# Kernel tuning notes

Hardware: AMD Instinct MI355X
Metric: run time of the kernel (lower is better)

Reference implementation:

```python
import jax, jax.numpy as jnp
import numpy as np

KSIZE = 8
STRIDE = 4
HEADS = 8
DIM_HEAD = 32
EPS = 1e-5


def _layernorm(x, g, b):
    m = jnp.mean(x, axis=-1, keepdims=True)
    v = jnp.mean(jnp.square(x - m), axis=-1, keepdims=True)
    return (x - m) / jnp.sqrt(v + EPS) * g + b


def setup_inputs() -> dict:
    key = jax.random.key(0)
    ks = jax.random.split(key, 4)
    B, H, W, C = 8, 64, 64, 256
    inner = HEADS * DIM_HEAD  # 256
    x = jax.random.normal(ks[0], (B, H, W, C), dtype=jnp.float32)
    return {
        "x": x,
        "ln1_g": jnp.ones((C,), jnp.float32),
        "ln1_b": jnp.zeros((C,), jnp.float32),
        "ln2_g": jnp.ones((C,), jnp.float32),
        "ln2_b": jnp.zeros((C,), jnp.float32),
        "w_qkv": jax.random.normal(ks[1], (C, inner * 3), jnp.float32) * 0.02,
        "w_out": jax.random.normal(ks[2], (inner, C), jnp.float32) * 0.02,
        "b_out": jnp.zeros((C,), jnp.float32),
    }


def reference(x, ln1_g, ln1_b, ln2_g, ln2_b, w_qkv, w_out, b_out):
    B, H, W, C = x.shape
    k, s = KSIZE, STRIDE
    nH = (H - k) // s + 1
    nW = (W - k) // s + 1
    L = nH * nW
    n = k * k  # tokens per window

    # window index grids (im2col / unfold)
    rows = jnp.arange(nH)[:, None] * s + jnp.arange(k)[None, :]  # [nH, k]
    cols = jnp.arange(nW)[:, None] * s + jnp.arange(k)[None, :]  # [nW, k]
    ridx = rows[:, None, :, None]  # [nH,1,k,1]
    cidx = cols[None, :, None, :]  # [1,nW,1,k]

    # unfold: [B, nH, nW, k, k, C] -> [(B L), (k k), C]
    patches = x[:, ridx, cidx, :].reshape(B * L, n, C)

    # LocalAttention2D.norm then AttentionBlock.norm
    p = _layernorm(patches, ln1_g, ln1_b)
    h = _layernorm(p, ln2_g, ln2_b)

    qkv = h @ w_qkv  # [(B L), n, 3*inner]
    q, kk, v = jnp.split(qkv, 3, axis=-1)
    q = q.reshape(B * L, n, HEADS, DIM_HEAD)
    kk = kk.reshape(B * L, n, HEADS, DIM_HEAD)
    v = v.reshape(B * L, n, HEADS, DIM_HEAD)

    scale = DIM_HEAD ** -0.5
    dots = jnp.einsum('bnhd,bmhd->bhnm', q, kk) * scale
    attn = jax.nn.softmax(dots, axis=-1)
    o = jnp.einsum('bhnm,bmhd->bnhd', attn, v).reshape(B * L, n, HEADS * DIM_HEAD)
    o = o @ w_out + b_out  # [(B L), n, C]

    # fold (col2im overlap-add)
    o = o.reshape(B, nH, nW, k, k, C)
    out = jnp.zeros((B, H, W, C), x.dtype).at[:, ridx, cidx, :].add(o)

    # normalization: fold(unfold(ones)) == overlap counts
    counts = jnp.zeros((H, W), x.dtype).at[ridx, cidx].add(1.0)
    return out / counts[None, :, :, None]
```

## Files before the change

### kernel.cpp

```cpp
#include <hip/hip_runtime.h>
#include <hip/hip_bf16.h>
#include <cstdint>
#include <cstddef>

#define LN_EPS 1e-5f
#define B_    8
#define HW_   64
#define C_    256
#define NTOK  (B_ * HW_ * HW_)
#define HEADS_ 8
#define DH_    32
#define NPATCH 15

__global__ __launch_bounds__(256) void ln_stats_kernel(
    const float* __restrict__ x, const float* __restrict__ g1,
    const float* __restrict__ b1, float4* __restrict__ stats)
{
    const int gid  = blockIdx.x * 256 + threadIdx.x;
    const int tok  = gid >> 6;
    const int lane = gid & 63;
    if (tok >= NTOK) return;
    const float4 xv = reinterpret_cast<const float4*>(x + (size_t)tok * C_)[lane];
    float s  = xv.x + xv.y + xv.z + xv.w;
    float sq = xv.x*xv.x + xv.y*xv.y + xv.z*xv.z + xv.w*xv.w;
    for (int off = 32; off; off >>= 1) {
        s  += __shfl_xor(s, off);
        sq += __shfl_xor(sq, off);
    }
    const float m1 = s * (1.0f / 256.0f);
    const float r1 = rsqrtf(fmaxf(sq * (1.0f / 256.0f) - m1 * m1, 0.0f) + LN_EPS);
    const float4 g = reinterpret_cast<const float4*>(g1)[lane];
    const float4 b = reinterpret_cast<const float4*>(b1)[lane];
    const float y0 = (xv.x - m1) * r1 * g.x + b.x;
    const float y1 = (xv.y - m1) * r1 * g.y + b.y;
    const float y2 = (xv.z - m1) * r1 * g.z + b.z;
    const float y3 = (xv.w - m1) * r1 * g.w + b.w;
    float s2  = y0 + y1 + y2 + y3;
    float sq2 = y0*y0 + y1*y1 + y2*y2 + y3*y3;
    for (int off = 32; off; off >>= 1) {
        s2  += __shfl_xor(s2, off);
        sq2 += __shfl_xor(sq2, off);
    }
    const float m2 = s2 * (1.0f / 256.0f);
    const float r2 = rsqrtf(fmaxf(sq2 * (1.0f / 256.0f) - m2 * m2, 0.0f) + LN_EPS);
    if (lane == 0) stats[tok] = make_float4(m1, r1, m2, r2);
}

__global__ __launch_bounds__(256) void qkv_kernel(
    const float* __restrict__ x, const float4* __restrict__ stats,
    const float* __restrict__ g1, const float* __restrict__ b1,
    const float* __restrict__ g2, const float* __restrict__ b2,
    const float* __restrict__ w, float* __restrict__ qkv)
{
    __shared__ float At[16][72];
    __shared__ float Bt[16][64];
    const int tid  = threadIdx.x;
    const int tok0 = blockIdx.y * 64;
    const int n0   = blockIdx.x * 64;
    const int ty = tid >> 4, tx = tid & 15;
    const int st = tid >> 2, sseg = tid & 3;
    const int bk = tid >> 4, bx = tid & 15;
    const float4 s4 = stats[tok0 + st];
    const float* xrow = x + (size_t)(tok0 + st) * C_;
    float acc[4][4] = {};
    for (int kk = 0; kk < 16; ++kk) {
        const int k0 = kk * 16;
        const int ka = k0 + sseg * 4;
        const float4 xv  = *reinterpret_cast<const float4*>(xrow + ka);
        const float4 g1v = *reinterpret_cast<const float4*>(g1 + ka);
        const float4 b1v = *reinterpret_cast<const float4*>(b1 + ka);
        const float4 g2v = *reinterpret_cast<const float4*>(g2 + ka);
        const float4 b2v = *reinterpret_cast<const float4*>(b2 + ka);
        const float h0 = ((xv.x - s4.x)*s4.y*g1v.x + b1v.x - s4.z)*s4.w*g2v.x + b2v.x;
        const float h1 = ((xv.y - s4.x)*s4.y*g1v.y + b1v.y - s4.z)*s4.w*g2v.y + b2v.y;
        const float h2 = ((xv.z - s4.x)*s4.y*g1v.z + b1v.z - s4.z)*s4.w*g2v.z + b2v.z;
        const float h3 = ((xv.w - s4.x)*s4.y*g1v.w + b1v.w - s4.z)*s4.w*g2v.w + b2v.w;
        const float4 wv = *reinterpret_cast<const float4*>(w + (size_t)(k0 + bk) * 768 + n0 + bx * 4);
        __syncthreads();
        At[sseg*4+0][st] = h0;
        At[sseg*4+1][st] = h1;
        At[sseg*4+2][st] = h2;
        At[sseg*4+3][st] = h3;
        *reinterpret_cast<float4*>(&Bt[bk][bx*4]) = wv;
        __syncthreads();
        #pragma unroll
        for (int k = 0; k < 16; ++k) {
            const float4 a = *reinterpret_cast<const float4*>(&At[k][ty*4]);
            const float4 b = *reinterpret_cast<const float4*>(&Bt[k][tx*4]);
            acc[0][0] += a.x*b.x; acc[0][1] += a.x*b.y; acc[0][2] += a.x*b.z; acc[0][3] += a.x*b.w;
            acc[1][0] += a.y*b.x; acc[1][1] += a.y*b.y; acc[1][2] += a.y*b.z; acc[1][3] += a.y*b.w;
            acc[2][0] += a.z*b.x; acc[2][1] += a.z*b.y; acc[2][2] += a.z*b.z; acc[2][3] += a.z*b.w;
            acc[3][0] += a.w*b.x; acc[3][1] += a.w*b.y; acc[3][2] += a.w*b.z; acc[3][3] += a.w*b.w;
        }
    }
    #pragma unroll
    for (int r = 0; r < 4; ++r) {
        const float4 o = make_float4(acc[r][0], acc[r][1], acc[r][2], acc[r][3]);
        *reinterpret_cast<float4*>(qkv + (size_t)(tok0 + ty*4 + r) * 768 + n0 + tx*4) = o;
    }
}

__global__ __launch_bounds__(256) void attn_o_kernel(
    const float* __restrict__ qkv, float* __restrict__ obuf)
{
    __shared__ float q_lds[64][36];
    __shared__ float kT[32][68];
    __shared__ float v_lds[64][36];
    __shared__ float p_lds[64][68];
    const int tid = threadIdx.x;
    const int b  = blockIdx.y;
    const int hd = blockIdx.z;
    const int pi = blockIdx.x / NPATCH;
    const int pj = blockIdx.x % NPATCH;
    const int t = tid >> 2, seg = tid & 3;
    const int pr = t >> 3, pc = t & 7;
    const size_t pixbase = ((size_t)((b * 64 + 4*pi + pr) * 64) + (4*pj + pc));
    {
        const size_t base = pixbase * 768 + hd * 32 + seg * 8;
        const float4 qa = *reinterpret_cast<const float4*>(qkv + base);
        const float4 qb = *reinterpret_cast<const float4*>(qkv + base + 4);
        const float4 ka = *reinterpret_cast<const float4*>(qkv + base + 256);
        const float4 kb = *reinterpret_cast<const float4*>(qkv + base + 260);
        const float4 va = *reinterpret_cast<const float4*>(qkv + base + 512);
        const float4 vb = *reinterpret_cast<const float4*>(qkv + base + 516);
        *reinterpret_cast<float4*>(&q_lds[t][seg*8    ]) = qa;
        *reinterpret_cast<float4*>(&q_lds[t][seg*8 + 4]) = qb;
        *reinterpret_cast<float4*>(&v_lds[t][seg*8    ]) = va;
        *reinterpret_cast<float4*>(&v_lds[t][seg*8 + 4]) = vb;
        const int d0 = seg * 8;
        kT[d0+0][t] = ka.x; kT[d0+1][t] = ka.y; kT[d0+2][t] = ka.z; kT[d0+3][t] = ka.w;
        kT[d0+4][t] = kb.x; kT[d0+5][t] = kb.y; kT[d0+6][t] = kb.z; kT[d0+7][t] = kb.w;
    }
    __syncthreads();
    const float scale = 0.17677669529663687f;
    const int tr = tid >> 4, tc = tid & 15;
    float s[4][4] = {};
    #pragma unroll
    for (int kk = 0; kk < 4; ++kk) {
        float qreg[4][8];
        #pragma unroll
        for (int i = 0; i < 4; ++i) {
            const float4 qv0 = *reinterpret_cast<const float4*>(&q_lds[tr*4 + i][kk*8]);
            const float4 qv1 = *reinterpret_cast<const float4*>(&q_lds[tr*4 + i][kk*8 + 4]);
            qreg[i][0] = qv0.x; qreg[i][1] = qv0.y; qreg[i][2] = qv0.z; qreg[i][3] = qv0.w;
            qreg[i][4] = qv1.x; qreg[i][5] = qv1.y; qreg[i][6] = qv1.z; qreg[i][7] = qv1.w;
        }
        #pragma unroll
        for (int w = 0; w < 8; ++w) {
            const float4 kv = *reinterpret_cast<const float4*>(&kT[kk*8 + w][tc*4]);
            const float ka[4] = {kv.x, kv.y, kv.z, kv.w};
            #pragma unroll
            for (int i = 0; i < 4; ++i) {
                #pragma unroll
                for (int j = 0; j < 4; ++j)
                    s[i][j] = fmaf(qreg[i][w], ka[j], s[i][j]);
            }
        }
    }
    float mrow[4], sum[4];
    #pragma unroll
    for (int i = 0; i < 4; ++i) {
        s[i][0] *= scale; s[i][1] *= scale; s[i][2] *= scale; s[i][3] *= scale;
        mrow[i] = fmaxf(fmaxf(s[i][0], s[i][1]), fmaxf(s[i][2], s[i][3]));
    }
    #pragma unroll
    for (int off = 1; off < 16; off <<= 1)
        #pragma unroll
        for (int i = 0; i < 4; ++i)
            mrow[i] = fmaxf(mrow[i], __shfl_xor(mrow[i], off));
    #pragma unroll
    for (int i = 0; i < 4; ++i) {
        sum[i] = 0.f;
        #pragma unroll
        for (int j = 0; j < 4; ++j) {
            s[i][j] = __expf(s[i][j] - mrow[i]);
            sum[i] += s[i][j];
        }
    }
    #pragma unroll
    for (int off = 1; off < 16; off <<= 1)
        #pragma unroll
        for (int i = 0; i < 4; ++i)
            sum[i] += __shfl_xor(sum[i], off);
    #pragma unroll
    for (int i = 0; i < 4; ++i) {
        const float rs = 1.0f / sum[i];
        #pragma unroll
        for (int j = 0; j < 4; ++j)
            p_lds[tr*4 + i][tc*4 + j] = s[i][j] * rs;
    }
    __syncthreads();
    float4 o0 = make_float4(0,0,0,0), o1 = make_float4(0,0,0,0);
    for (int jc = 0; jc < 64; ++jc) {
        const float a = p_lds[t][jc];
        const float4 v0 = *reinterpret_cast<const float4*>(&v_lds[jc][seg*8]);
        const float4 v1 = *reinterpret_cast<const float4*>(&v_lds[jc][seg*8 + 4]);
        o0.x = fmaf(a, v0.x, o0.x); o0.y = fmaf(a, v0.y, o0.y);
        o0.z = fmaf(a, v0.z, o0.z); o0.w = fmaf(a, v0.w, o0.w);
        o1.x = fmaf(a, v1.x, o1.x); o1.y = fmaf(a, v1.y, o1.y);
        o1.z = fmaf(a, v1.z, o1.z); o1.w = fmaf(a, v1.w, o1.w);
    }
    float* op = obuf + ((size_t)(b * 225 + pi * NPATCH + pj) * 64 + t) * 256 + hd * 32 + seg * 8;
    *reinterpret_cast<float4*>(op)     = o0;
    *reinterpret_cast<float4*>(op + 4) = o1;
}

__global__ __launch_bounds__(256) void proj_gather_kernel(
    const float* __restrict__ obuf, const float* __restrict__ w,
    const float* __restrict__ bo, float* __restrict__ out)
{
    __shared__ float At[16][36];
    __shared__ float Bt[16][256];
    const int tid  = threadIdx.x;
    const int tok0 = blockIdx.x * 32;
    const int ty = tid >> 5, tx = tid & 31;
    const int st = tid >> 2, sseg = tid & 3;
    const int bc = (tid & 63) * 4, bkb = tid >> 6;
    const float* s00 = obuf; const float* s01 = obuf;
    const float* s10 = obuf; const float* s11 = obuf;
    if (tid < 128) {
        const int token = tok0 + st;
        const int bb = token >> 12;
        const int hp = (token >> 6) & 63, wp = token & 63;
        const int pil = (hp >= 4) ? ((hp - 4) >> 2) : 0;
        const int pih = (hp >> 2) > 14 ? 14 : (hp >> 2);
        const int pjl = (wp >= 4) ? ((wp - 4) >> 2) : 0;
        const int pjh = (wp >> 2) > 14 ? 14 : (wp >> 2);
        const size_t base_b = (size_t)bb * 225;
        s00 = obuf + ((base_b + pil * NPATCH + pjl) * 64 + (8*(hp-4*pil) + (wp-4*pjl))) * 256;
        s01 = obuf + ((base_b + pil * NPATCH + pjh) * 64 + (8*(hp-4*pil) + (wp-4*pjh))) * 256;
        s10 = obuf + ((base_b + pih * NPATCH + pjl) * 64 + (8*(hp-4*pih) + (wp-4*pjl))) * 256;
        s11 = obuf + ((base_b + pih * NPATCH + pjh) * 64 + (8*(hp-4*pih) + (wp-4*pjh))) * 256;
    }
    float acc[4][8] = {};
    for (int kk = 0; kk < 16; ++kk) {
        const int k0 = kk * 16;
        float4 av = make_float4(0,0,0,0);
        if (tid < 128) {
            const int off = k0 + sseg * 4;
            const float4 v0 = *reinterpret_cast<const float4*>(s00 + off);
            const float4 v1 = *reinterpret_cast<const float4*>(s01 + off);
            const float4 v2 = *reinterpret_cast<const float4*>(s10 + off);
            const float4 v3 = *reinterpret_cast<const float4*>(s11 + off);
            av.x = ((v0.x + v1.x) + (v2.x + v3.x)) * 0.25f;
            av.y = ((v0.y + v1.y) + (v2.y + v3.y)) * 0.25f;
            av.z = ((v0.z + v1.z) + (v2.z + v3.z)) * 0.25f;
            av.w = ((v0.w + v1.w) + (v2.w + v3.w)) * 0.25f;
        }
        float4 wv[4];
        #pragma unroll
        for (int u = 0; u < 4; ++u)
            wv[u] = *reinterpret_cast<const float4*>(w + (size_t)(k0 + bkb*4 + u) * 256 + bc);
        __syncthreads();
        if (tid < 128) {
            At[sseg*4+0][st] = av.x;
            At[sseg*4+1][st] = av.y;
            At[sseg*4+2][st] = av.z;
            At[sseg*4+3][st] = av.w;
        }
        #pragma unroll
        for (int u = 0; u < 4; ++u)
            *reinterpret_cast<float4*>(&Bt[bkb*4+u][bc]) = wv[u];
        __syncthreads();
        #pragma unroll
        for (int k = 0; k < 16; ++k) {
            const float4 a  = *reinterpret_cast<const float4*>(&At[k][ty*4]);
            const float4 b0 = *reinterpret_cast<const float4*>(&Bt[k][tx*4]);
            const float4 b1 = *reinterpret_cast<const float4*>(&Bt[k][128 + tx*4]);
            acc[0][0] += a.x*b0.x; acc[0][1] += a.x*b0.y; acc[0][2] += a.x*b0.z; acc[0][3] += a.x*b0.w;
            acc[0][4] += a.x*b1.x; acc[0][5] += a.x*b1.y; acc[0][6] += a.x*b1.z; acc[0][7] += a.x*b1.w;
            acc[1][0] += a.y*b0.x; acc[1][1] += a.y*b0.y; acc[1][2] += a.y*b0.z; acc[1][3] += a.y*b0.w;
            acc[1][4] += a.y*b1.x; acc[1][5] += a.y*b1.y; acc[1][6] += a.y*b1.z; acc[1][7] += a.y*b1.w;
            acc[2][0] += a.z*b0.x; acc[2][1] += a.z*b0.y; acc[2][2] += a.z*b0.z; acc[2][3] += a.z*b0.w;
            acc[2][4] += a.z*b1.x; acc[2][5] += a.z*b1.y; acc[2][6] += a.z*b1.z; acc[2][7] += a.z*b1.w;
            acc[3][0] += a.w*b0.x; acc[3][1] += a.w*b0.y; acc[3][2] += a.w*b0.z; acc[3][3] += a.w*b0.w;
            acc[3][4] += a.w*b1.x; acc[3][5] += a.w*b1.y; acc[3][6] += a.w*b1.z; acc[3][7] += a.w*b1.w;
        }
    }
    const float4 bo0 = *reinterpret_cast<const float4*>(bo + tx*4);
    const float4 bo1 = *reinterpret_cast<const float4*>(bo + 128 + tx*4);
    #pragma unroll
    for (int r = 0; r < 4; ++r) {
        float* orow = out + (size_t)(tok0 + ty*4 + r) * 256;
        const float4 o0 = make_float4(acc[r][0]+bo0.x, acc[r][1]+bo0.y, acc[r][2]+bo0.z, acc[r][3]+bo0.w);
        const float4 o1 = make_float4(acc[r][4]+bo1.x, acc[r][5]+bo1.y, acc[r][6]+bo1.z, acc[r][7]+bo1.w);
        *reinterpret_cast<float4*>(orow + tx*4)       = o0;
        *reinterpret_cast<float4*>(orow + 128 + tx*4) = o1;
    }
}

__global__ __launch_bounds__(256) void attn_kernel(
    const float* __restrict__ qkv, float* __restrict__ out,
    int gi, int gj, int nJ, int do_store)
{
    __shared__ float q_lds[64][36];
    __shared__ float kT[32][68];
    __shared__ float v_lds[64][36];
    __shared__ float p_lds[64][68];
    const int tid = threadIdx.x;
    const int b  = blockIdx.y;
    const int hd = blockIdx.z;
    const int pi = 2 * (blockIdx.x / nJ) + gi;
    const int pj = 2 * (blockIdx.x % nJ) + gj;
    const int t = tid >> 2, seg = tid & 3;
    const int pr = t >> 3, pc = t & 7;
    const size_t pixbase = ((size_t)((b * 64 + 4*pi + pr) * 64) + (4*pj + pc));
    {
        const size_t base = pixbase * 768 + hd * 32 + seg * 8;
        const float4 qa = *reinterpret_cast<const float4*>(qkv + base);
        const float4 qb = *reinterpret_cast<const float4*>(qkv + base + 4);
        const float4 ka = *reinterpret_cast<const float4*>(qkv + base + 256);
        const float4 kb = *reinterpret_cast<const float4*>(qkv + base + 260);
        const float4 va = *reinterpret_cast<const float4*>(qkv + base + 512);
        const float4 vb = *reinterpret_cast<const float4*>(qkv + base + 516);
        *reinterpret_cast<float4*>(&q_lds[t][seg*8    ]) = qa;
        *reinterpret_cast<float4*>(&q_lds[t][seg*8 + 4]) = qb;
        *reinterpret_cast<float4*>(&v_lds[t][seg*8    ]) = va;
        *reinterpret_cast<float4*>(&v_lds[t][seg*8 + 4]) = vb;
        const int d0 = seg * 8;
        kT[d0+0][t] = ka.x; kT[d0+1][t] = ka.y; kT[d0+2][t] = ka.z; kT[d0+3][t] = ka.w;
        kT[d0+4][t] = kb.x; kT[d0+5][t] = kb.y; kT[d0+6][t] = kb.z; kT[d0+7][t] = kb.w;
    }
    __syncthreads();
    const float scale = 0.17677669529663687f;
    const int tr = tid >> 4, tc = tid & 15;
    float s[4][4] = {};
    #pragma unroll
    for (int kk = 0; kk < 4; ++kk) {
        float qreg[4][8];
        #pragma unroll
        for (int i = 0; i < 4; ++i) {
            const float4 qv0 = *reinterpret_cast<const float4*>(&q_lds[tr*4 + i][kk*8]);
            const float4 qv1 = *reinterpret_cast<const float4*>(&q_lds[tr*4 + i][kk*8 + 4]);
            qreg[i][0] = qv0.x; qreg[i][1] = qv0.y; qreg[i][2] = qv0.z; qreg[i][3] = qv0.w;
            qreg[i][4] = qv1.x; qreg[i][5] = qv1.y; qreg[i][6] = qv1.z; qreg[i][7] = qv1.w;
        }
        #pragma unroll
        for (int w = 0; w < 8; ++w) {
            const float4 kv = *reinterpret_cast<const float4*>(&kT[kk*8 + w][tc*4]);
            const float ka[4] = {kv.x, kv.y, kv.z, kv.w};
            #pragma unroll
            for (int i = 0; i < 4; ++i) {
                #pragma unroll
                for (int j = 0; j < 4; ++j)
                    s[i][j] = fmaf(qreg[i][w], ka[j], s[i][j]);
            }
        }
    }
    float mrow[4], sum[4];
    #pragma unroll
    for (int i = 0; i < 4; ++i) {
        s[i][0] *= scale; s[i][1] *= scale; s[i][2] *= scale; s[i][3] *= scale;
        mrow[i] = fmaxf(fmaxf(s[i][0], s[i][1]), fmaxf(s[i][2], s[i][3]));
    }
    #pragma unroll
    for (int off = 1; off < 16; off <<= 1)
        #pragma unroll
        for (int i = 0; i < 4; ++i)
            mrow[i] = fmaxf(mrow[i], __shfl_xor(mrow[i], off));
    #pragma unroll
    for (int i = 0; i < 4; ++i) {
        sum[i] = 0.f;
        #pragma unroll
        for (int j = 0; j < 4; ++j) {
            s[i][j] = __expf(s[i][j] - mrow[i]);
            sum[i] += s[i][j];
        }
    }
    #pragma unroll
    for (int off = 1; off < 16; off <<= 1)
        #pragma unroll
        for (int i = 0; i < 4; ++i)
            sum[i] += __shfl_xor(sum[i], off);
    #pragma unroll
    for (int i = 0; i < 4; ++i) {
        const float rs = 1.0f / sum[i];
        #pragma unroll
        for (int j = 0; j < 4; ++j)
            p_lds[tr*4 + i][tc*4 + j] = s[i][j] * rs;
    }
    __syncthreads();
    float4 o0 = make_float4(0,0,0,0), o1 = make_float4(0,0,0,0);
    for (int jc = 0; jc < 64; ++jc) {
        const float a = p_lds[t][jc];
        const float4 v0 = *reinterpret_cast<const float4*>(&v_lds[jc][seg*8]);
        const float4 v1 = *reinterpret_cast<const float4*>(&v_lds[jc][seg*8 + 4]);
        o0.x = fmaf(a, v0.x, o0.x); o0.y = fmaf(a, v0.y, o0.y);
        o0.z = fmaf(a, v0.z, o0.z); o0.w = fmaf(a, v0.w, o0.w);
        o1.x = fmaf(a, v1.x, o1.x); o1.y = fmaf(a, v1.y, o1.y);
        o1.z = fmaf(a, v1.z, o1.z); o1.w = fmaf(a, v1.w, o1.w);
    }
    float* op = out + pixbase * 256 + hd * 32 + seg * 8;
    if (do_store) {
        *reinterpret_cast<float4*>(op)     = o0;
        *reinterpret_cast<float4*>(op + 4) = o1;
    } else {
        float4 c0 = *reinterpret_cast<const float4*>(op);
        float4 c1 = *reinterpret_cast<const float4*>(op + 4);
        c0.x += o0.x; c0.y += o0.y; c0.z += o0.z; c0.w += o0.w;
        c1.x += o1.x; c1.y += o1.y; c1.z += o1.z; c1.w += o1.w;
        *reinterpret_cast<float4*>(op)     = c0;
        *reinterpret_cast<float4*>(op + 4) = c1;
    }
}

__global__ __launch_bounds__(256) void proj_kernel(
    float* __restrict__ out, const float* __restrict__ w, const float* __restrict__ bo)
{
    __shared__ float At[16][36];
    __shared__ float Bt[16][256];
    const int tid  = threadIdx.x;
    const int tok0 = blockIdx.x * 32;
    const int ty = tid >> 5, tx = tid & 31;
    const int st = tid >> 2, sseg = tid & 3;
    const int bc = (tid & 63) * 4, bkb = tid >> 6;
    float ascale = 0.f;
    if (tid < 128) {
        const int token = tok0 + st;
        const int hp = (token >> 6) & 63, wp = token & 63;
        const float cnt = ((hp >= 4 && hp < 60) ? 2.f : 1.f) * ((wp >= 4 && wp < 60) ? 2.f : 1.f);
        ascale = 1.0f / cnt;
    }
    float acc[4][8] = {};
    for (int kk = 0; kk < 16; ++kk) {
        const int k0 = kk * 16;
        float4 av = make_float4(0,0,0,0);
        if (tid < 128)
            av = *reinterpret_cast<const float4*>(out + (size_t)(tok0 + st) * 256 + k0 + sseg * 4);
        float4 wv[4];
        #pragma unroll
        for (int u = 0; u < 4; ++u)
            wv[u] = *reinterpret_cast<const float4*>(w + (size_t)(k0 + bkb*4 + u) * 256 + bc);
        __syncthreads();
        if (tid < 128) {
            At[sseg*4+0][st] = av.x * ascale;
            At[sseg*4+1][st] = av.y * ascale;
            At[sseg*4+2][st] = av.z * ascale;
            At[sseg*4+3][st] = av.w * ascale;
        }
        #pragma unroll
        for (int u = 0; u < 4; ++u)
            *reinterpret_cast<float4*>(&Bt[bkb*4+u][bc]) = wv[u];
        __syncthreads();
        #pragma unroll
        for (int k = 0; k < 16; ++k) {
            const float4 a  = *reinterpret_cast<const float4*>(&At[k][ty*4]);
            const float4 b0 = *reinterpret_cast<const float4*>(&Bt[k][tx*4]);
            const float4 b1 = *reinterpret_cast<const float4*>(&Bt[k][128 + tx*4]);
            acc[0][0] += a.x*b0.x; acc[0][1] += a.x*b0.y; acc[0][2] += a.x*b0.z; acc[0][3] += a.x*b0.w;
            acc[0][4] += a.x*b1.x; acc[0][5] += a.x*b1.y; acc[0][6] += a.x*b1.z; acc[0][7] += a.x*b1.w;
            acc[1][0] += a.y*b0.x; acc[1][1] += a.y*b0.y; acc[1][2] += a.y*b0.z; acc[1][3] += a.y*b0.w;
            acc[1][4] += a.y*b1.x; acc[1][5] += a.y*b1.y; acc[1][6] += a.y*b1.z; acc[1][7] += a.y*b1.w;
            acc[2][0] += a.z*b0.x; acc[2][1] += a.z*b0.y; acc[2][2] += a.z*b0.z; acc[2][3] += a.z*b0.w;
            acc[2][4] += a.z*b1.x; acc[2][5] += a.z*b1.y; acc[2][6] += a.z*b1.z; acc[2][7] += a.z*b1.w;
            acc[3][0] += a.w*b0.x; acc[3][1] += a.w*b0.y; acc[3][2] += a.w*b0.z; acc[3][3] += a.w*b0.w;
            acc[3][4] += a.w*b1.x; acc[3][5] += a.w*b1.y; acc[3][6] += a.w*b1.z; acc[3][7] += a.w*b1.w;
        }
    }
    const float4 bo0 = *reinterpret_cast<const float4*>(bo + tx*4);
    const float4 bo1 = *reinterpret_cast<const float4*>(bo + 128 + tx*4);
    #pragma unroll
    for (int r = 0; r < 4; ++r) {
        float* orow = out + (size_t)(tok0 + ty*4 + r) * 256;
        const float4 o0 = make_float4(acc[r][0]+bo0.x, acc[r][1]+bo0.y, acc[r][2]+bo0.z, acc[r][3]+bo0.w);
        const float4 o1 = make_float4(acc[r][4]+bo1.x, acc[r][5]+bo1.y, acc[r][6]+bo1.z, acc[r][7]+bo1.w);
        *reinterpret_cast<float4*>(orow + tx*4)       = o0;
        *reinterpret_cast<float4*>(orow + 128 + tx*4) = o1;
    }
}

extern "C" void kernel_launch(void* const* d_in, const int* in_sizes, int n_in,
                              void* d_out, int out_size, void* d_ws, size_t ws_size,
                              hipStream_t stream)
{
    const float* x     = (const float*)d_in[0];
    const float* ln1_g = (const float*)d_in[1];
    const float* ln1_b = (const float*)d_in[2];
    const float* ln2_g = (const float*)d_in[3];
    const float* ln2_b = (const float*)d_in[4];
    const float* w_qkv = (const float*)d_in[5];
    const float* w_out = (const float*)d_in[6];
    const float* b_out = (const float*)d_in[7];
    float* out = (float*)d_out;
    char*  ws  = (char*)d_ws;

    const size_t stats_b = (size_t)NTOK * 16;
    const size_t qkv_b   = (size_t)NTOK * 768 * 4;
    const size_t obuf_b  = (size_t)B_ * 225 * 64 * 256 * 4;

    float4* stats = (float4*)ws;
    float*  qkv   = (float*)(ws + stats_b);
    float*  obuf  = (float*)(ws + stats_b + qkv_b);

    ln_stats_kernel<<<NTOK / 4, 256, 0, stream>>>(x, ln1_g, ln1_b, stats);
    qkv_kernel<<<dim3(12, NTOK / 64), 256, 0, stream>>>(
        x, stats, ln1_g, ln1_b, ln2_g, ln2_b, w_qkv, qkv);

    if (ws_size >= stats_b + qkv_b + obuf_b) {
        attn_o_kernel<<<dim3(225, B_, HEADS_), 256, 0, stream>>>(qkv, obuf);
        proj_gather_kernel<<<NTOK / 32, 256, 0, stream>>>(obuf, w_out, b_out, out);
    } else {
        for (int g = 0; g < 4; ++g) {
            const int gi = g >> 1, gj = g & 1;
            const int nI = gi ? 7 : 8, nJ = gj ? 7 : 8;
            attn_kernel<<<dim3(nI * nJ, B_, HEADS_), 256, 0, stream>>>(
                qkv, out, gi, gj, nJ, (g == 0) ? 1 : 0);
        }
        proj_kernel<<<NTOK / 32, 256, 0, stream>>>(out, w_out, b_out);
    }
}
```

Before: 463.8 us.

## Materialize double-layernormed activations before QKV GEMM and alias attention LDS buffers

Adds a kernel that applies both layernorms and writes the normalized activations to a workspace buffer, so the QKV GEMM becomes a plain tiled GEMM instead of recomputing normalization while loading its tiles. The attention kernels now reuse the Q/K region of shared memory for the probability matrix, with an extra barrier, which shrinks LDS per block and may raise occupancy. The cost is an extra full write and read of a 32 MB activation tensor and a larger workspace requirement. A fallback keeps the old path when the workspace is too small.

After: 456.2 us. Within noise of the previous version (-1.6%).

```diff
diff --git a/kernel.cpp b/kernel.cpp
--- a/kernel.cpp
+++ b/kernel.cpp
@@ -11,6 +11,89 @@
 #define HEADS_ 8
 #define DH_    32
 #define NPATCH 15
+
+__global__ __launch_bounds__(256) void ln_h_kernel(
+    const float* __restrict__ x, const float* __restrict__ g1,
+    const float* __restrict__ b1, const float* __restrict__ g2,
+    const float* __restrict__ b2, float* __restrict__ h)
+{
+    const int gid  = blockIdx.x * 256 + threadIdx.x;
+    const int tok  = gid >> 6;
+    const int lane = gid & 63;
+    if (tok >= NTOK) return;
+    const float4 xv = reinterpret_cast<const float4*>(x + (size_t)tok * C_)[lane];
+    float s  = xv.x + xv.y + xv.z + xv.w;
+    float sq = xv.x*xv.x + xv.y*xv.y + xv.z*xv.z + xv.w*xv.w;
+    for (int off = 32; off; off >>= 1) {
+        s  += __shfl_xor(s, off);
+        sq += __shfl_xor(sq, off);
+    }
+    const float m1 = s * (1.0f / 256.0f);
+    const float r1 = rsqrtf(fmaxf(sq * (1.0f / 256.0f) - m1 * m1, 0.0f) + LN_EPS);
+    const float4 g = reinterpret_cast<const float4*>(g1)[lane];
+    const float4 b = reinterpret_cast<const float4*>(b1)[lane];
+    const float y0 = (xv.x - m1) * r1 * g.x + b.x;
+    const float y1 = (xv.y - m1) * r1 * g.y + b.y;
+    const float y2 = (xv.z - m1) * r1 * g.z + b.z;
+    const float y3 = (xv.w - m1) * r1 * g.w + b.w;
+    float s2  = y0 + y1 + y2 + y3;
+    float sq2 = y0*y0 + y1*y1 + y2*y2 + y3*y3;
+    for (int off = 32; off; off >>= 1) {
+        s2  += __shfl_xor(s2, off);
+        sq2 += __shfl_xor(sq2, off);
+    }
+    const float m2 = s2 * (1.0f / 256.0f);
+    const float r2 = rsqrtf(fmaxf(sq2 * (1.0f / 256.0f) - m2 * m2, 0.0f) + LN_EPS);
+    const float4 G = reinterpret_cast<const float4*>(g2)[lane];
+    const float4 B = reinterpret_cast<const float4*>(b2)[lane];
+    float4 hv;
+    hv.x = (y0 - m2) * r2 * G.x + B.x;
+    hv.y = (y1 - m2) * r2 * G.y + B.y;
+    hv.z = (y2 - m2) * r2 * G.z + B.z;
+    hv.w = (y3 - m2) * r2 * G.w + B.w;
+    reinterpret_cast<float4*>(h + (size_t)tok * C_)[lane] = hv;
+}
+
+__global__ __launch_bounds__(256) void qkv_h_kernel(
+    const float* __restrict__ h, const float* __restrict__ w, float* __restrict__ qkv)
+{
+    __shared__ float At[16][76];
+    __shared__ float Bt[16][64];
+    const int tid  = threadIdx.x;
+    const int tok0 = blockIdx.y * 64;
+    const int n0   = blockIdx.x * 64;
+    const int ty = tid >> 4, tx = tid & 15;
+    const int st = tid >> 2, sseg = tid & 3;
+    const int bk = tid >> 4, bxn = tid & 15;
+    const float* hrow = h + (size_t)(tok0 + st) * C_;
+    float acc[4][4] = {};
+    for (int kk = 0; kk < 16; ++kk) {
+        const int k0 = kk * 16;
+        const float4 hv = *reinterpret_cast<const float4*>(hrow + k0 + sseg * 4);
+        const float4 wv = *reinterpret_cast<const float4*>(w + (size_t)(k0 + bk) * 768 + n0 + bxn * 4);
+        __syncthreads();
+        At[sseg*4+0][st] = hv.x;
+        At[sseg*4+1][st] = hv.y;
+        At[sseg*4+2][st] = hv.z;
+        At[sseg*4+3][st] = hv.w;
+        *reinterpret_cast<float4*>(&Bt[bk][bxn*4]) = wv;
+        __syncthreads();
+        #pragma unroll
+        for (int k = 0; k < 16; ++k) {
+            const float4 a = *reinterpret_cast<const float4*>(&At[k][ty*4]);
+            const float4 b = *reinterpret_cast<const float4*>(&Bt[k][tx*4]);
+            acc[0][0] += a.x*b.x; acc[0][1] += a.x*b.y; acc[0][2] += a.x*b.z; acc[0][3] += a.x*b.w;
+            acc[1][0] += a.y*b.x; acc[1][1] += a.y*b.y; acc[1][2] += a.y*b.z; acc[1][3] += a.y*b.w;
+            acc[2][0] += a.z*b.x; acc[2][1] += a.z*b.y; acc[2][2] += a.z*b.z; acc[2][3] += a.z*b.w;
+            acc[3][0] += a.w*b.x; acc[3][1] += a.w*b.y; acc[3][2] += a.w*b.z; acc[3][3] += a.w*b.w;
+        }
+    }
+    #pragma unroll
+    for (int r = 0; r < 4; ++r) {
+        const float4 o = make_float4(acc[r][0], acc[r][1], acc[r][2], acc[r][3]);
+        *reinterpret_cast<float4*>(qkv + (size_t)(tok0 + ty*4 + r) * 768 + n0 + tx*4) = o;
+    }
+}
 
 __global__ __launch_bounds__(256) void ln_stats_kernel(
     const float* __restrict__ x, const float* __restrict__ g1,
@@ -103,10 +186,11 @@
 __global__ __launch_bounds__(256) void attn_o_kernel(
     const float* __restrict__ qkv, float* __restrict__ obuf)
 {
-    __shared__ float q_lds[64][36];
-    __shared__ float kT[32][68];
-    __shared__ float v_lds[64][36];
-    __shared__ float p_lds[64][68];
+    __shared__ float smem[6784];
+    float (*q_lds)[36] = reinterpret_cast<float(*)[36]>(smem);
+    float (*kT)[68]    = reinterpret_cast<float(*)[68]>(smem + 2304);
+    float (*v_lds)[36] = reinterpret_cast<float(*)[36]>(smem + 4480);
+    float (*p_lds)[67] = reinterpret_cast<float(*)[67]>(smem);
     const int tid = threadIdx.x;
     const int b  = blockIdx.y;
     const int hd = blockIdx.z;
@@ -182,6 +266,7 @@
         #pragma unroll
         for (int i = 0; i < 4; ++i)
             sum[i] += __shfl_xor(sum[i], off);
+    __syncthreads();
     #pragma unroll
     for (int i = 0; i < 4; ++i) {
         const float rs = 1.0f / sum[i];
@@ -205,98 +290,15 @@
     *reinterpret_cast<float4*>(op + 4) = o1;
 }
 
-__global__ __launch_bounds__(256) void proj_gather_kernel(
-    const float* __restrict__ obuf, const float* __restrict__ w,
-    const float* __restrict__ bo, float* __restrict__ out)
-{
-    __shared__ float At[16][36];
-    __shared__ float Bt[16][256];
-    const int tid  = threadIdx.x;
-    const int tok0 = blockIdx.x * 32;
-    const int ty = tid >> 5, tx = tid & 31;
-    const int st = tid >> 2, sseg = tid & 3;
-    const int bc = (tid & 63) * 4, bkb = tid >> 6;
-    const float* s00 = obuf; const float* s01 = obuf;
-    const float* s10 = obuf; const float* s11 = obuf;
-    if (tid < 128) {
-        const int token = tok0 + st;
-        const int bb = token >> 12;
-        const int hp = (token >> 6) & 63, wp = token & 63;
-        const int pil = (hp >= 4) ? ((hp - 4) >> 2) : 0;
-        const int pih = (hp >> 2) > 14 ? 14 : (hp >> 2);
-        const int pjl = (wp >= 4) ? ((wp - 4) >> 2) : 0;
-        const int pjh = (wp >> 2) > 14 ? 14 : (wp >> 2);
-        const size_t base_b = (size_t)bb * 225;
-        s00 = obuf + ((base_b + pil * NPATCH + pjl) * 64 + (8*(hp-4*pil) + (wp-4*pjl))) * 256;
-        s01 = obuf + ((base_b + pil * NPATCH + pjh) * 64 + (8*(hp-4*pil) + (wp-4*pjh))) * 256;
-        s10 = obuf + ((base_b + pih * NPATCH + pjl) * 64 + (8*(hp-4*pih) + (wp-4*pjl))) * 256;
-        s11 = obuf + ((base_b + pih * NPATCH + pjh) * 64 + (8*(hp-4*pih) + (wp-4*pjh))) * 256;
-    }
-    float acc[4][8] = {};
-    for (int kk = 0; kk < 16; ++kk) {
-        const int k0 = kk * 16;
-        float4 av = make_float4(0,0,0,0);
-        if (tid < 128) {
-            const int off = k0 + sseg * 4;
-            const float4 v0 = *reinterpret_cast<const float4*>(s00 + off);
-            const float4 v1 = *reinterpret_cast<const float4*>(s01 + off);
-            const float4 v2 = *reinterpret_cast<const float4*>(s10 + off);
-            const float4 v3 = *reinterpret_cast<const float4*>(s11 + off);
-            av.x = ((v0.x + v1.x) + (v2.x + v3.x)) * 0.25f;
-            av.y = ((v0.y + v1.y) + (v2.y + v3.y)) * 0.25f;
-            av.z = ((v0.z + v1.z) + (v2.z + v3.z)) * 0.25f;
-            av.w = ((v0.w + v1.w) + (v2.w + v3.w)) * 0.25f;
-        }
-        float4 wv[4];
-        #pragma unroll
-        for (int u = 0; u < 4; ++u)
-            wv[u] = *reinterpret_cast<const float4*>(w + (size_t)(k0 + bkb*4 + u) * 256 + bc);
-        __syncthreads();
-        if (tid < 128) {
-            At[sseg*4+0][st] = av.x;
-            At[sseg*4+1][st] = av.y;
-            At[sseg*4+2][st] = av.z;
-            At[sseg*4+3][st] = av.w;
-        }
-        #pragma unroll
-        for (int u = 0; u < 4; ++u)
-            *reinterpret_cast<float4*>(&Bt[bkb*4+u][bc]) = wv[u];
-        __syncthreads();
-        #pragma unroll
-        for (int k = 0; k < 16; ++k) {
-            const float4 a  = *reinterpret_cast<const float4*>(&At[k][ty*4]);
-            const float4 b0 = *reinterpret_cast<const float4*>(&Bt[k][tx*4]);
-            const float4 b1 = *reinterpret_cast<const float4*>(&Bt[k][128 + tx*4]);
-            acc[0][0] += a.x*b0.x; acc[0][1] += a.x*b0.y; acc[0][2] += a.x*b0.z; acc[0][3] += a.x*b0.w;
-            acc[0][4] += a.x*b1.x; acc[0][5] += a.x*b1.y; acc[0][6] += a.x*b1.z; acc[0][7] += a.x*b1.w;
-            acc[1][0] += a.y*b0.x; acc[1][1] += a.y*b0.y; acc[1][2] += a.y*b0.z; acc[1][3] += a.y*b0.w;
-            acc[1][4] += a.y*b1.x; acc[1][5] += a.y*b1.y; acc[1][6] += a.y*b1.z; acc[1][7] += a.y*b1.w;
-            acc[2][0] += a.z*b0.x; acc[2][1] += a.z*b0.y; acc[2][2] += a.z*b0.z; acc[2][3] += a.z*b0.w;
-            acc[2][4] += a.z*b1.x; acc[2][5] += a.z*b1.y; acc[2][6] += a.z*b1.z; acc[2][7] += a.z*b1.w;
-            acc[3][0] += a.w*b0.x; acc[3][1] += a.w*b0.y; acc[3][2] += a.w*b0.z; acc[3][3] += a.w*b0.w;
-            acc[3][4] += a.w*b1.x; acc[3][5] += a.w*b1.y; acc[3][6] += a.w*b1.z; acc[3][7] += a.w*b1.w;
-        }
-    }
-    const float4 bo0 = *reinterpret_cast<const float4*>(bo + tx*4);
-    const float4 bo1 = *reinterpret_cast<const float4*>(bo + 128 + tx*4);
-    #pragma unroll
-    for (int r = 0; r < 4; ++r) {
-        float* orow = out + (size_t)(tok0 + ty*4 + r) * 256;
-        const float4 o0 = make_float4(acc[r][0]+bo0.x, acc[r][1]+bo0.y, acc[r][2]+bo0.z, acc[r][3]+bo0.w);
-        const float4 o1 = make_float4(acc[r][4]+bo1.x, acc[r][5]+bo1.y, acc[r][6]+bo1.z, acc[r][7]+bo1.w);
-        *reinterpret_cast<float4*>(orow + tx*4)       = o0;
-        *reinterpret_cast<float4*>(orow + 128 + tx*4) = o1;
-    }
-}
-
 __global__ __launch_bounds__(256) void attn_kernel(
     const float* __restrict__ qkv, float* __restrict__ out,
     int gi, int gj, int nJ, int do_store)
 {
-    __shared__ float q_lds[64][36];
-    __shared__ float kT[32][68];
-    __shared__ float v_lds[64][36];
-    __shared__ float p_lds[64][68];
+    __shared__ float smem[6784];
+    float (*q_lds)[36] = reinterpret_cast<float(*)[36]>(smem);
+    float (*kT)[68]    = reinterpret_cast<float(*)[68]>(smem + 2304);
+    float (*v_lds)[36] = reinterpret_cast<float(*)[36]>(smem + 4480);
+    float (*p_lds)[67] = reinterpret_cast<float(*)[67]>(smem);
     const int tid = threadIdx.x;
     const int b  = blockIdx.y;
     const int hd = blockIdx.z;
@@ -372,6 +374,7 @@
         #pragma unroll
         for (int i = 0; i < 4; ++i)
             sum[i] += __shfl_xor(sum[i], off);
+    __syncthreads();
     #pragma unroll
     for (int i = 0; i < 4; ++i) {
         const float rs = 1.0f / sum[i];
@@ -401,6 +404,90 @@
         c1.x += o1.x; c1.y += o1.y; c1.z += o1.z; c1.w += o1.w;
         *reinterpret_cast<float4*>(op)     = c0;
         *reinterpret_cast<float4*>(op + 4) = c1;
+    }
+}
+
+__global__ __launch_bounds__(256) void proj_gather_kernel(
+    const float* __restrict__ obuf, const float* __restrict__ w,
+    const float* __restrict__ bo, float* __restrict__ out)
+{
+    __shared__ float At[16][36];
+    __shared__ float Bt[16][256];
+    const int tid  = threadIdx.x;
+    const int tok0 = blockIdx.x * 32;
+    const int ty = tid >> 5, tx = tid & 31;
+    const int st = tid >> 2, sseg = tid & 3;
+    const int bc = (tid & 63) * 4, bkb = tid >> 6;
+    const float* s00 = obuf; const float* s01 = obuf;
+    const float* s10 = obuf; const float* s11 = obuf;
+    if (tid < 128) {
+        const int token = tok0 + st;
+        const int bb = token >> 12;
+        const int hp = (token >> 6) & 63, wp = token & 63;
+        const int pil = (hp >= 4) ? ((hp - 4) >> 2) : 0;
+        const int pih = (hp >> 2) > 14 ? 14 : (hp >> 2);
+        const int pjl = (wp >= 4) ? ((wp - 4) >> 2) : 0;
+        const int pjh = (wp >> 2) > 14 ? 14 : (wp >> 2);
+        const size_t base_b = (size_t)bb * 225;
+        s00 = obuf + ((base_b + pil * NPATCH + pjl) * 64 + (8*(hp-4*pil) + (wp-4*pjl))) * 256;
+        s01 = obuf + ((base_b + pil * NPATCH + pjh) * 64 + (8*(hp-4*pil) + (wp-4*pjh))) * 256;
+        s10 = obuf + ((base_b + pih * NPATCH + pjl) * 64 + (8*(hp-4*pih) + (wp-4*pjl))) * 256;
+        s11 = obuf + ((base_b + pih * NPATCH + pjh) * 64 + (8*(hp-4*pih) + (wp-4*pjh))) * 256;
+    }
+    float acc[4][8] = {};
+    for (int kk = 0; kk < 16; ++kk) {
+        const int k0 = kk * 16;
+        float4 av = make_float4(0,0,0,0);
+        if (tid < 128) {
+            const int off = k0 + sseg * 4;
+            const float4 v0 = *reinterpret_cast<const float4*>(s00 + off);
+            const float4 v1 = *reinterpret_cast<const float4*>(s01 + off);
+            const float4 v2 = *reinterpret_cast<const float4*>(s10 + off);
+            const float4 v3 = *reinterpret_cast<const float4*>(s11 + off);
+            av.x = ((v0.x + v1.x) + (v2.x + v3.x)) * 0.25f;
+            av.y = ((v0.y + v1.y) + (v2.y + v3.y)) * 0.25f;
+            av.z = ((v0.z + v1.z) + (v2.z + v3.z)) * 0.25f;
+            av.w = ((v0.w + v1.w) + (v2.w + v3.w)) * 0.25f;
+        }
+        float4 wv[4];
+        #pragma unroll
+        for (int u = 0; u < 4; ++u)
+            wv[u] = *reinterpret_cast<const float4*>(w + (size_t)(k0 + bkb*4 + u) * 256 + bc);
+        __syncthreads();
+        if (tid < 128) {
+            At[sseg*4+0][st] = av.x;
+            At[sseg*4+1][st] = av.y;
+            At[sseg*4+2][st] = av.z;
+            At[sseg*4+3][st] = av.w;
+        }
+        #pragma unroll
+        for (int u = 0; u < 4; ++u)
+            *reinterpret_cast<float4*>(&Bt[bkb*4+u][bc]) = wv[u];
+        __syncthreads();
+        #pragma unroll
+        for (int k = 0; k < 16; ++k) {
+            const float4 a  = *reinterpret_cast<const float4*>(&At[k][ty*4]);
+            const float4 b0 = *reinterpret_cast<const float4*>(&Bt[k][tx*4]);
+            const float4 b1 = *reinterpret_cast<const float4*>(&Bt[k][128 + tx*4]);
+            acc[0][0] += a.x*b0.x; acc[0][1] += a.x*b0.y; acc[0][2] += a.x*b0.z; acc[0][3] += a.x*b0.w;
+            acc[0][4] += a.x*b1.x; acc[0][5] += a.x*b1.y; acc[0][6] += a.x*b1.z; acc[0][7] += a.x*b1.w;
+            acc[1][0] += a.y*b0.x; acc[1][1] += a.y*b0.y; acc[1][2] += a.y*b0.z; acc[1][3] += a.y*b0.w;
+            acc[1][4] += a.y*b1.x; acc[1][5] += a.y*b1.y; acc[1][6] += a.y*b1.z; acc[1][7] += a.y*b1.w;
+            acc[2][0] += a.z*b0.x; acc[2][1] += a.z*b0.y; acc[2][2] += a.z*b0.z; acc[2][3] += a.z*b0.w;
+            acc[2][4] += a.z*b1.x; acc[2][5] += a.z*b1.y; acc[2][6] += a.z*b1.z; acc[2][7] += a.z*b1.w;
+            acc[3][0] += a.w*b0.x; acc[3][1] += a.w*b0.y; acc[3][2] += a.w*b0.z; acc[3][3] += a.w*b0.w;
+            acc[3][4] += a.w*b1.x; acc[3][5] += a.w*b1.y; acc[3][6] += a.w*b1.z; acc[3][7] += a.w*b1.w;
+        }
+    }
+    const float4 bo0 = *reinterpret_cast<const float4*>(bo + tx*4);
+    const float4 bo1 = *reinterpret_cast<const float4*>(bo + 128 + tx*4);
+    #pragma unroll
+    for (int r = 0; r < 4; ++r) {
+        float* orow = out + (size_t)(tok0 + ty*4 + r) * 256;
+        const float4 o0 = make_float4(acc[r][0]+bo0.x, acc[r][1]+bo0.y, acc[r][2]+bo0.z, acc[r][3]+bo0.w);
+        const float4 o1 = make_float4(acc[r][4]+bo1.x, acc[r][5]+bo1.y, acc[r][6]+bo1.z, acc[r][7]+bo1.w);
+        *reinterpret_cast<float4*>(orow + tx*4)       = o0;
+        *reinterpret_cast<float4*>(orow + 128 + tx*4) = o1;
     }
 }
 
@@ -484,22 +571,35 @@
     float* out = (float*)d_out;
     char*  ws  = (char*)d_ws;
 
+    const size_t h_b    = (size_t)NTOK * C_ * 4;
+    const size_t qkv_b  = (size_t)NTOK * 768 * 4;
+    const size_t obuf_b = (size_t)B_ * 225 * 64 * 256 * 4;
     const size_t stats_b = (size_t)NTOK * 16;
-    const size_t qkv_b   = (size_t)NTOK * 768 * 4;
-    const size_t obuf_b  = (size_t)B_ * 225 * 64 * 256 * 4;
-
-    float4* stats = (float4*)ws;
-    float*  qkv   = (float*)(ws + stats_b);
-    float*  obuf  = (float*)(ws + stats_b + qkv_b);
-
-    ln_stats_kernel<<<NTOK / 4, 256, 0, stream>>>(x, ln1_g, ln1_b, stats);
-    qkv_kernel<<<dim3(12, NTOK / 64), 256, 0, stream>>>(
-        x, stats, ln1_g, ln1_b, ln2_g, ln2_b, w_qkv, qkv);
-
-    if (ws_size >= stats_b + qkv_b + obuf_b) {
-        attn_o_kernel<<<dim3(225, B_, HEADS_), 256, 0, stream>>>(qkv, obuf);
-        proj_gather_kernel<<<NTOK / 32, 256, 0, stream>>>(obuf, w_out, b_out, out);
+
+    if (ws_size >= h_b + qkv_b) {
+        float* h    = (float*)ws;
+        float* qkv  = (float*)(ws + h_b);
+        float* obuf = (float*)(ws + h_b + qkv_b);
+        ln_h_kernel<<<NTOK / 4, 256, 0, stream>>>(x, ln1_g, ln1_b, ln2_g, ln2_b, h);
+        qkv_h_kernel<<<dim3(12, NTOK / 64), 256, 0, stream>>>(h, w_qkv, qkv);
+        if (ws_size >= h_b + qkv_b + obuf_b) {
+            attn_o_kernel<<<dim3(225, B_, HEADS_), 256, 0, stream>>>(qkv, obuf);
+            proj_gather_kernel<<<NTOK / 32, 256, 0, stream>>>(obuf, w_out, b_out, out);
+        } else {
+            for (int g = 0; g < 4; ++g) {
+                const int gi = g >> 1, gj = g & 1;
+                const int nI = gi ? 7 : 8, nJ = gj ? 7 : 8;
+                attn_kernel<<<dim3(nI * nJ, B_, HEADS_), 256, 0, stream>>>(
+                    qkv, out, gi, gj, nJ, (g == 0) ? 1 : 0);
+            }
+            proj_kernel<<<NTOK / 32, 256, 0, stream>>>(out, w_out, b_out);
+        }
     } else {
+        float4* stats = (float4*)ws;
+        float*  qkv   = (float*)(ws + stats_b);
+        ln_stats_kernel<<<NTOK / 4, 256, 0, stream>>>(x, ln1_g, ln1_b, stats);
+        qkv_kernel<<<dim3(12, NTOK / 64), 256, 0, stream>>>(
+            x, stats, ln1_g, ln1_b, ln2_g, ln2_b, w_qkv, qkv);
         for (int g = 0; g < 4; ++g) {
             const int gi = g >> 1, gj = g & 1;
             const int nI = gi ? 7 : 8, nJ = gj ? 7 : 8;
```
